# Optimization experiments

Hardware: AMD Instinct MI355X
Metric: run time of the kernel (lower is better)

## Reference

```python
import jax, jax.numpy as jnp
import numpy as np

N_HEADS = 16
HEAD_DIM = 64
HIDDEN = 1024


def setup_inputs() -> dict:
    key = jax.random.key(0)
    kx, kq, kk, kv, ko = jax.random.split(key, 5)
    B, S = 1, 4096
    # xavier_uniform for Linear(hidden, n_heads*head_dim): limit = sqrt(6/(fan_in+fan_out))
    lim = float(np.sqrt(6.0 / (HIDDEN + N_HEADS * HEAD_DIM)))
    x = jax.random.normal(kx, (B, S, HIDDEN), dtype=jnp.float32)
    wq = jax.random.uniform(kq, (N_HEADS * HEAD_DIM, HIDDEN), jnp.float32, -lim, lim)
    wk = jax.random.uniform(kk, (N_HEADS * HEAD_DIM, HIDDEN), jnp.float32, -lim, lim)
    wv = jax.random.uniform(kv, (N_HEADS * HEAD_DIM, HIDDEN), jnp.float32, -lim, lim)
    wo = jax.random.uniform(ko, (HIDDEN, N_HEADS * HEAD_DIM), jnp.float32, -lim, lim)
    return {"x": x, "wq": wq, "wk": wk, "wv": wv, "wo": wo}


def reference(x, wq, wk, wv, wo):
    B, S, _ = x.shape
    scale = HEAD_DIM ** -0.5
    # project and split heads: [B, H, S, D]
    def proj(w):
        return jnp.einsum('bsh,eh->bse', x, w).reshape(B, S, N_HEADS, HEAD_DIM).transpose(0, 2, 1, 3)
    q, k, v = proj(wq), proj(wk), proj(wv)
    scores = jnp.einsum('bhqd,bhkd->bhqk', q, k) * scale  # [B,H,S,S]
    causal = jnp.tril(jnp.ones((S, S), dtype=bool))
    scores = jnp.where(causal, scores, -jnp.inf)
    probs = jax.nn.softmax(scores, axis=-1)
    out = jnp.einsum('bhqk,bhkd->bhqd', probs, v)  # [B,H,S,D]
    out = out.transpose(0, 2, 1, 3).reshape(B, S, N_HEADS * HEAD_DIM)
    return jnp.einsum('bse,he->bsh', out, wo)
```

## Files before the change

kernel.cpp:

```cpp
#include <hip/hip_runtime.h>
#include <hip/hip_bf16.h>
#include <stdint.h>

typedef unsigned short u16;
typedef float f32x4 __attribute__((ext_vector_type(4)));
typedef __bf16 bf16x8 __attribute__((ext_vector_type(8)));
typedef u16 u16x8 __attribute__((ext_vector_type(8)));

#define GL2LDS16(g, l)                                                          \
  __builtin_amdgcn_global_load_lds(                                             \
      (const __attribute__((address_space(1))) unsigned int*)(g),               \
      (__attribute__((address_space(3))) unsigned int*)(l), 16, 0, 0)

#if __has_builtin(__builtin_amdgcn_exp2f)
#define EXP2(x) __builtin_amdgcn_exp2f(x)
#else
#define EXP2(x) exp2f(x)
#endif

__device__ __forceinline__ u16 f2bf(float f) {
  uint32_t u = __builtin_bit_cast(uint32_t, f);
  return (u16)((u + 0x7FFFu + ((u >> 16) & 1u)) >> 16);
}

__device__ __forceinline__ uint32_t cvt_pk_bf16(float lo, float hi) {
  uint32_t r;
  asm("v_cvt_pk_bf16_f32 %0, %1, %2" : "=v"(r) : "v"(lo), "v"(hi));
  return r;
}

__device__ __forceinline__ void cast8(const float* __restrict__ s,
                                      u16* __restrict__ d) {
  const float4* p = (const float4*)s;
  float4 a = p[0], b = p[1];
  uint4 o;
  o.x = cvt_pk_bf16(a.x, a.y);
  o.y = cvt_pk_bf16(a.z, a.w);
  o.z = cvt_pk_bf16(b.x, b.y);
  o.w = cvt_pk_bf16(b.z, b.w);
  *(uint4*)d = o;
}

__global__ __launch_bounds__(256) void cast_kernel(const float* __restrict__ s,
                                                   u16* __restrict__ d, int n) {
  int i = (blockIdx.x * 256 + threadIdx.x) * 8;
  if (i >= n) return;
  cast8(s + i, d + i);
}

__global__ __launch_bounds__(256) void cast4_kernel(const float* __restrict__ s0,
                                                    const float* __restrict__ s1,
                                                    const float* __restrict__ s2,
                                                    const float* __restrict__ s3,
                                                    u16* __restrict__ d) {
  int b = blockIdx.x >> 9;
  int i = ((blockIdx.x & 511) * 256 + threadIdx.x) * 8;
  const float* s = (b == 0) ? s0 : (b == 1) ? s1 : (b == 2) ? s2 : s3;
  cast8(s + i, d + ((size_t)b << 20) + i);
}

template <typename CT>
__global__ __launch_bounds__(256) void gemm_bt(const u16* __restrict__ A,
                                               const u16* __restrict__ B,
                                               CT* __restrict__ C, int M, int N,
                                               int K) {
  __shared__ u16 As[128 * 32];
  __shared__ u16 Bs[128 * 32];
  const int tid = threadIdx.x;
  const int lane = tid & 63;
  const int l15 = lane & 15, lhi = lane >> 4;
  const int wave = tid >> 6;
  const int wr = (wave >> 1) * 64, wc = (wave & 1) * 64;
  const int m0 = blockIdx.y * 128, n0 = blockIdx.x * 128;

  f32x4 acc[4][4] = {};

  for (int k0 = 0; k0 < K; k0 += 32) {
    __syncthreads();
#pragma unroll
    for (int i = 0; i < 2; ++i) {
      int c = tid + i * 256;
      int row = c >> 2, slot = c & 3;
      int scol = (slot ^ ((row >> 1) & 3)) * 8;
      GL2LDS16(A + (size_t)(m0 + row) * K + k0 + scol, (char*)As + c * 16);
      GL2LDS16(B + (size_t)(n0 + row) * K + k0 + scol, (char*)Bs + c * 16);
    }
    __syncthreads();
    bf16x8 af[4], bfr[4];
#pragma unroll
    for (int mi = 0; mi < 4; ++mi) {
      int row = wr + mi * 16 + l15;
      int byt = row * 64 + ((lhi ^ ((row >> 1) & 3)) << 4);
      af[mi] = *(const bf16x8*)((const char*)As + byt);
    }
#pragma unroll
    for (int ni = 0; ni < 4; ++ni) {
      int row = wc + ni * 16 + l15;
      int byt = row * 64 + ((lhi ^ ((row >> 1) & 3)) << 4);
      bfr[ni] = *(const bf16x8*)((const char*)Bs + byt);
    }
#pragma unroll
    for (int mi = 0; mi < 4; ++mi)
#pragma unroll
      for (int ni = 0; ni < 4; ++ni)
        acc[mi][ni] = __builtin_amdgcn_mfma_f32_16x16x32_bf16(
            af[mi], bfr[ni], acc[mi][ni], 0, 0, 0);
  }

#pragma unroll
  for (int mi = 0; mi < 4; ++mi) {
    int rbase = m0 + wr + mi * 16 + lhi * 4;
#pragma unroll
    for (int ni = 0; ni < 4; ++ni) {
      int col = n0 + wc + ni * 16 + l15;
#pragma unroll
      for (int r = 0; r < 4; ++r) {
        float v = acc[mi][ni][r];
        if constexpr (sizeof(CT) == 2)
          C[(size_t)(rbase + r) * N + col] = (CT)f2bf(v);
        else
          C[(size_t)(rbase + r) * N + col] = v;
      }
    }
  }
}

__global__ __launch_bounds__(256) void vtrans_kernel(const u16* __restrict__ qkv,
                                                     u16* __restrict__ vt) {
  __shared__ u16 t[64][72];
  const int bs = blockIdx.x * 64;
  const int be = blockIdx.y * 64;
  const int tid = threadIdx.x;
#pragma unroll
  for (int i = 0; i < 2; ++i) {
    int c = tid + i * 256, row = c >> 3, col = (c & 7) * 8;
    *(u16x8*)&t[row][col] =
        *(const u16x8*)(qkv + (size_t)(bs + row) * 3072 + 2048 + be + col);
  }
  __syncthreads();
#pragma unroll
  for (int i = 0; i < 2; ++i) {
    int c = tid + i * 256, erow = c >> 3, scol = (c & 7) * 8;
    u16x8 o;
#pragma unroll
    for (int j = 0; j < 8; ++j) o[j] = t[scol + j][erow];
    *(u16x8*)(vt + (size_t)(be + erow) * 4096 + bs + scol) = o;
  }
}

__global__ __launch_bounds__(256) void attn_kernel(const u16* __restrict__ qkv,
                                                   const u16* __restrict__ vt,
                                                   u16* __restrict__ out) {
  const int h = blockIdx.y;
  const int bx = blockIdx.x;
  const int tid = threadIdx.x;
  const int lane = tid & 63, wave = tid >> 6;
  const int l15 = lane & 15, lhi = lane >> 4;

  __shared__ u16 Ks[2][64 * 64];
  __shared__ u16 Vs[2][64 * 64];
  __shared__ u16 Ps[4][16 * 64];
  u16* Pw = Ps[wave];

  const float SC = 0.18033688f;

  int koff[2][4];
#pragma unroll
  for (int ks = 0; ks < 2; ++ks)
#pragma unroll
    for (int nf = 0; nf < 4; ++nf) {
      int row = nf * 16 + l15;
      koff[ks][nf] = row * 128 + ((lhi * 16 + ks * 64) ^ ((row & 7) << 4));
    }
  int poff[4];
#pragma unroll
  for (int nf = 0; nf < 4; ++nf)
    poff[nf] = l15 * 128 + ((nf * 32 + lhi * 8) ^ ((l15 & 7) << 4));

  auto stage = [&](int b, int kb) {
#pragma unroll
    for (int i = 0; i < 2; ++i) {
      int c = tid + i * 256;
      int row = c >> 3, slot = c & 7;
      int scol = (slot ^ (row & 7)) * 8;
      GL2LDS16(qkv + (size_t)(kb * 64 + row) * 3072 + 1024 + h * 64 + scol,
               (char*)(Ks[b]) + c * 16);
      GL2LDS16(vt + (size_t)(h * 64 + row) * 4096 + kb * 64 + scol,
               (char*)(Vs[b]) + c * 16);
    }
  };

  int cur = 0;
  for (int rep = 0; rep < 2; ++rep) {
    const int qb = rep ? (63 - bx) : bx;
    const int q0 = qb * 64 + wave * 16;
    const u16* Qb = qkv + (size_t)(q0 + l15) * 3072 + h * 64;
    bf16x8 qf0 = *(const bf16x8*)(const void*)(Qb + lhi * 8);
    bf16x8 qf1 = *(const bf16x8*)(const void*)(Qb + 32 + lhi * 8);

    f32x4 oa[4] = {};
    float mrow = -1e30f, lrow = 0.f;

    stage(cur, 0);
    asm volatile("s_waitcnt vmcnt(0)" ::: "memory");
    __builtin_amdgcn_s_barrier();

    for (int kb = 0; kb <= qb; ++kb) {
      if (kb < qb) stage(cur ^ 1, kb + 1);

      f32x4 s[4] = {};
#pragma unroll
      for (int ks = 0; ks < 2; ++ks)
#pragma unroll
        for (int nf = 0; nf < 4; ++nf) {
          bf16x8 kf =
              *(const bf16x8*)((const char*)(Ks[cur]) + koff[ks][nf]);
          s[nf] = __builtin_amdgcn_mfma_f32_16x16x32_bf16(kf, ks ? qf1 : qf0,
                                                          s[nf], 0, 0, 0);
        }

      if (kb == qb) {
        const int qloc = wave * 16 + l15;
#pragma unroll
        for (int nf = 0; nf < 4; ++nf)
#pragma unroll
          for (int r = 0; r < 4; ++r) {
            float v = s[nf][r] * SC;
            if (nf * 16 + lhi * 4 + r > qloc) v = -1e30f;
            s[nf][r] = v;
          }
      } else {
#pragma unroll
        for (int nf = 0; nf < 4; ++nf)
#pragma unroll
          for (int r = 0; r < 4; ++r) s[nf][r] *= SC;
      }

      float pm0 = fmaxf(fmaxf(s[0][0], s[0][1]), fmaxf(s[0][2], s[0][3]));
      float pm1 = fmaxf(fmaxf(s[1][0], s[1][1]), fmaxf(s[1][2], s[1][3]));
      float pm2 = fmaxf(fmaxf(s[2][0], s[2][1]), fmaxf(s[2][2], s[2][3]));
      float pm3 = fmaxf(fmaxf(s[3][0], s[3][1]), fmaxf(s[3][2], s[3][3]));
      float pm = fmaxf(fmaxf(pm0, pm1), fmaxf(pm2, pm3));
      pm = fmaxf(pm, __shfl_xor(pm, 16));
      pm = fmaxf(pm, __shfl_xor(pm, 32));

      if (__any(pm - mrow > 8.0f)) {
        float mn = fmaxf(mrow, pm);
        float al = EXP2(mrow - mn);
        mrow = mn;
        lrow *= al;
        float alq[4];
#pragma unroll
        for (int r = 0; r < 4; ++r) alq[r] = __shfl(al, lhi * 4 + r, 16);
#pragma unroll
        for (int nf = 0; nf < 4; ++nf)
#pragma unroll
          for (int r = 0; r < 4; ++r) oa[nf][r] *= alq[r];
      }

#pragma unroll
      for (int nf = 0; nf < 4; ++nf)
#pragma unroll
        for (int r = 0; r < 4; ++r) s[nf][r] = EXP2(s[nf][r] - mrow);
      float rs = ((s[0][0] + s[0][1]) + (s[0][2] + s[0][3])) +
                 ((s[1][0] + s[1][1]) + (s[1][2] + s[1][3])) +
                 ((s[2][0] + s[2][1]) + (s[2][2] + s[2][3])) +
                 ((s[3][0] + s[3][1]) + (s[3][2] + s[3][3]));
      rs += __shfl_xor(rs, 16);
      rs += __shfl_xor(rs, 32);
      lrow += rs;

#pragma unroll
      for (int nf = 0; nf < 4; ++nf) {
        uint2 pk;
        pk.x = cvt_pk_bf16(s[nf][0], s[nf][1]);
        pk.y = cvt_pk_bf16(s[nf][2], s[nf][3]);
        *(uint2*)((char*)Pw + poff[nf]) = pk;
      }

      bf16x8 pf[2];
#pragma unroll
      for (int ks = 0; ks < 2; ++ks)
        pf[ks] = *(const bf16x8*)((const char*)Pw + koff[ks][0]);

#pragma unroll
      for (int ks = 0; ks < 2; ++ks)
#pragma unroll
        for (int nf = 0; nf < 4; ++nf) {
          bf16x8 vf =
              *(const bf16x8*)((const char*)(Vs[cur]) + koff[ks][nf]);
          oa[nf] = __builtin_amdgcn_mfma_f32_16x16x32_bf16(pf[ks], vf, oa[nf],
                                                           0, 0, 0);
        }

      asm volatile("s_waitcnt vmcnt(0)" ::: "memory");
      __builtin_amdgcn_s_barrier();
      cur ^= 1;
    }

    float linv[4];
#pragma unroll
    for (int r = 0; r < 4; ++r)
      linv[r] = 1.0f / __shfl(lrow, lhi * 4 + r, 16);
#pragma unroll
    for (int r = 0; r < 4; ++r) {
      int rowg = q0 + lhi * 4 + r;
#pragma unroll
      for (int nf = 0; nf < 4; ++nf)
        out[(size_t)rowg * 1024 + h * 64 + nf * 16 + l15] =
            f2bf(oa[nf][r] * linv[r]);
    }
  }
}

extern "C" void kernel_launch(void* const* d_in, const int* in_sizes, int n_in,
                              void* d_out, int out_size, void* d_ws,
                              size_t ws_size, hipStream_t stream) {
  const float* x = (const float*)d_in[0];
  const float* wq = (const float*)d_in[1];
  const float* wk = (const float*)d_in[2];
  const float* wv = (const float*)d_in[3];
  const float* wo = (const float*)d_in[4];

  u16* xb = (u16*)d_ws;
  u16* wqkv = xb + 4096 * 1024;
  u16* wob = wqkv + 3072 * 1024;
  u16* qkv = wob + 1024 * 1024;
  u16* atn = qkv + (size_t)4096 * 3072;
  u16* vt = xb;

  cast_kernel<<<2048, 256, 0, stream>>>(x, xb, 4096 * 1024);
  cast4_kernel<<<2048, 256, 0, stream>>>(wq, wk, wv, wo, wqkv);

  gemm_bt<u16><<<dim3(24, 32), 256, 0, stream>>>(xb, wqkv, qkv, 4096, 3072, 1024);
  vtrans_kernel<<<dim3(64, 16), 256, 0, stream>>>(qkv, vt);
  attn_kernel<<<dim3(32, 16), 256, 0, stream>>>(qkv, vt, atn);
  gemm_bt<float><<<dim3(8, 32), 256, 0, stream>>>(atn, wob, (float*)d_out, 4096,
                                                  1024, 1024);
}
```

Measured before the change: 243.8 us.

## Use 256x256 double-buffered GEMM for QKV projection and fold softmax scale into Q

Replaces the 128x128 QKV projection GEMM with a new 512-thread kernel that uses 256x256 tiles and a K-step of 64. It double-buffers LDS with direct global-to-LDS loads interleaved among the MFMA phases and raises wave priority around the MFMA blocks. The softmax scale is applied to the Q columns in the GEMM epilogue, which removes the per-element multiply from the attention inner loop. The larger tiles raise LDS use to 128KB per block and launch only 192 blocks, which may underfill the GPU's compute units.

```diff
diff --git a/kernel.cpp b/kernel.cpp
--- a/kernel.cpp
+++ b/kernel.cpp
@@ -17,6 +17,8 @@
 #else
 #define EXP2(x) exp2f(x)
 #endif
+
+#define SOFTMAX_SC 0.18033688f
 
 __device__ __forceinline__ u16 f2bf(float f) {
   uint32_t u = __builtin_bit_cast(uint32_t, f);
@@ -57,6 +59,106 @@
   int i = ((blockIdx.x & 511) * 256 + threadIdx.x) * 8;
   const float* s = (b == 0) ? s0 : (b == 1) ? s1 : (b == 2) ? s2 : s3;
   cast8(s + i, d + ((size_t)b << 20) + i);
+}
+
+__global__ __launch_bounds__(512, 2) void gemm8(const u16* __restrict__ A,
+                                                const u16* __restrict__ B,
+                                                u16* __restrict__ C, int M,
+                                                int N, int K, int scaleq) {
+  __shared__ u16 As[2][256 * 64];
+  __shared__ u16 Bs[2][256 * 64];
+  const int tid = threadIdx.x;
+  const int lane = tid & 63;
+  const int l15 = lane & 15, lhi = lane >> 4;
+  const int wave = tid >> 6;
+  const int wm = wave >> 2, wn = wave & 3;
+  const int m0 = blockIdx.y * 256, n0 = blockIdx.x * 256;
+  const int nt = K >> 6;
+
+  int aoff[2][8], boff[2][4];
+#pragma unroll
+  for (int ks = 0; ks < 2; ++ks) {
+    int sl = ((ks * 4 + lhi) ^ (l15 & 7)) << 4;
+#pragma unroll
+    for (int m = 0; m < 8; ++m)
+      aoff[ks][m] = (wm * 128 + m * 16 + l15) * 128 + sl;
+#pragma unroll
+    for (int n = 0; n < 4; ++n)
+      boff[ks][n] = (wn * 64 + n * 16 + l15) * 128 + sl;
+  }
+
+  auto unit = [&](int b, int t, int u) {
+    const u16* src = (u < 2) ? A : B;
+    const int base = ((u < 2) ? m0 : n0) + (u & 1) * 128;
+    u16* lb = ((u < 2) ? As[b] : Bs[b]) + (u & 1) * 128 * 64;
+#pragma unroll
+    for (int i = 0; i < 2; ++i) {
+      int c = tid + i * 512;
+      int row = c >> 3, slot = c & 7;
+      int scol = (slot ^ (row & 7)) * 8;
+      GL2LDS16(src + (size_t)(base + row) * K + t * 64 + scol,
+               (char*)lb + c * 16);
+    }
+  };
+
+  f32x4 acc[8][4] = {};
+
+#pragma unroll
+  for (int u = 0; u < 4; ++u) unit(0, 0, u);
+  asm volatile("s_waitcnt vmcnt(0)" ::: "memory");
+  __builtin_amdgcn_s_barrier();
+
+  int cur = 0;
+  for (int t = 0; t < nt; ++t) {
+    const bool pre = (t + 1) < nt;
+    const char* Ab = (const char*)As[cur];
+    const char* Bb = (const char*)Bs[cur];
+    bf16x8 af[4], bfr[4];
+
+#pragma unroll
+    for (int p = 0; p < 4; ++p) {
+      const int ks = p >> 1, mh = p & 1;
+#pragma unroll
+      for (int j = 0; j < 4; ++j)
+        af[j] = *(const bf16x8*)(Ab + aoff[ks][mh * 4 + j]);
+      if (mh == 0) {
+#pragma unroll
+        for (int n = 0; n < 4; ++n)
+          bfr[n] = *(const bf16x8*)(Bb + boff[ks][n]);
+      }
+      if (p < 2 && pre) {
+        unit(cur ^ 1, t + 1, p * 2);
+        unit(cur ^ 1, t + 1, p * 2 + 1);
+      }
+      __builtin_amdgcn_s_barrier();
+      asm volatile("s_waitcnt lgkmcnt(0)" ::: "memory");
+      __builtin_amdgcn_sched_barrier(0);
+      __builtin_amdgcn_s_setprio(1);
+#pragma unroll
+      for (int j = 0; j < 4; ++j)
+#pragma unroll
+        for (int n = 0; n < 4; ++n)
+          acc[mh * 4 + j][n] = __builtin_amdgcn_mfma_f32_16x16x32_bf16(
+              af[j], bfr[n], acc[mh * 4 + j][n], 0, 0, 0);
+      __builtin_amdgcn_s_setprio(0);
+      if (p == 3) asm volatile("s_waitcnt vmcnt(0)" ::: "memory");
+      __builtin_amdgcn_s_barrier();
+    }
+    cur ^= 1;
+  }
+
+#pragma unroll
+  for (int m = 0; m < 8; ++m) {
+    int rbase = m0 + wm * 128 + m * 16 + lhi * 4;
+#pragma unroll
+    for (int n = 0; n < 4; ++n) {
+      int col = n0 + wn * 64 + n * 16 + l15;
+      float sc = (scaleq && col < 1024) ? SOFTMAX_SC : 1.0f;
+#pragma unroll
+      for (int r = 0; r < 4; ++r)
+        C[(size_t)(rbase + r) * N + col] = f2bf(acc[m][n][r] * sc);
+    }
+  }
 }
 
 template <typename CT>
@@ -162,8 +264,6 @@
   __shared__ u16 Ps[4][16 * 64];
   u16* Pw = Ps[wave];
 
-  const float SC = 0.18033688f;
-
   int koff[2][4];
 #pragma unroll
   for (int ks = 0; ks < 2; ++ks)
@@ -224,16 +324,8 @@
 #pragma unroll
         for (int nf = 0; nf < 4; ++nf)
 #pragma unroll
-          for (int r = 0; r < 4; ++r) {
-            float v = s[nf][r] * SC;
-            if (nf * 16 + lhi * 4 + r > qloc) v = -1e30f;
-            s[nf][r] = v;
-          }
-      } else {
-#pragma unroll
-        for (int nf = 0; nf < 4; ++nf)
-#pragma unroll
-          for (int r = 0; r < 4; ++r) s[nf][r] *= SC;
+          for (int r = 0; r < 4; ++r)
+            if (nf * 16 + lhi * 4 + r > qloc) s[nf][r] = -1e30f;
       }
 
       float pm0 = fmaxf(fmaxf(s[0][0], s[0][1]), fmaxf(s[0][2], s[0][3]));
@@ -332,7 +424,7 @@
   cast_kernel<<<2048, 256, 0, stream>>>(x, xb, 4096 * 1024);
   cast4_kernel<<<2048, 256, 0, stream>>>(wq, wk, wv, wo, wqkv);
 
-  gemm_bt<u16><<<dim3(24, 32), 256, 0, stream>>>(xb, wqkv, qkv, 4096, 3072, 1024);
+  gemm8<<<dim3(12, 16), 512, 0, stream>>>(xb, wqkv, qkv, 4096, 3072, 1024, 1);
   vtrans_kernel<<<dim3(64, 16), 256, 0, stream>>>(qkv, vt);
   attn_kernel<<<dim3(32, 16), 256, 0, stream>>>(qkv, vt, atn);
   gemm_bt<float><<<dim3(8, 32), 256, 0, stream>>>(atn, wob, (float*)d_out, 4096,
```

Result: no change. 242.6 us (-0.5%).
